# Kernel optimization log

Hardware: AMD Instinct MI355X
Metric: run time of the kernel (lower is better)

The kernel has to match this reference:

```python
import jax, jax.numpy as jnp
import numpy as np

HEADS = 4


def setup_inputs() -> dict:
    key = jax.random.key(0)
    kx, kqkv, kbq, ko, kbo = jax.random.split(key, 5)
    B, C, H, W = 4, 256, 64, 64
    x = jax.random.normal(kx, (B, C, H, W), dtype=jnp.float32)
    # torch nn.Linear stores weight as [out_features, in_features]
    w_qkv = jax.random.normal(kqkv, (3 * C, C), dtype=jnp.float32) * (1.0 / np.sqrt(C))
    b_qkv = jax.random.normal(kbq, (3 * C,), dtype=jnp.float32) * 0.02
    w_o = jax.random.normal(ko, (C, C), dtype=jnp.float32) * (1.0 / np.sqrt(C))
    b_o = jax.random.normal(kbo, (C,), dtype=jnp.float32) * 0.02
    return {"x": x, "w_qkv": w_qkv, "b_qkv": b_qkv, "w_o": w_o, "b_o": b_o}


def reference(x, w_qkv, b_qkv, w_o, b_o):
    B, C, H, W = x.shape
    S = H * W
    hd = C // HEADS
    # (B, C, H, W) -> (B, S, C)
    xt = x.reshape(B, C, S).transpose(0, 2, 1)
    qkv = xt @ w_qkv.T + b_qkv                      # (B, S, 3C)
    q, k, v = jnp.split(qkv, 3, axis=-1)
    def to_heads(t):
        return t.reshape(B, S, HEADS, hd).transpose(0, 2, 1, 3)  # (B, h, S, hd)
    q, k, v = to_heads(q), to_heads(k), to_heads(v)
    scores = jnp.einsum('bhqd,bhkd->bhqk', q, k) / jnp.sqrt(jnp.float32(hd))
    attn = jax.nn.softmax(scores, axis=-1)          # dropout inactive (eval)
    out = jnp.einsum('bhqk,bhkd->bhqd', attn, v)    # (B, h, S, hd)
    out = out.transpose(0, 2, 1, 3).reshape(B, S, C)
    y = out @ w_o.T + b_o                            # (B, S, C)
    y = y.reshape(B, H, W, C).transpose(0, 3, 1, 2)  # (B, C, H, W)
    return y
```

## Files before the change

### kernel.cpp

```cpp
#include <hip/hip_runtime.h>
#include <stdint.h>

#define DI __device__ __forceinline__

typedef __attribute__((ext_vector_type(8))) __bf16 bf16x8;
typedef __attribute__((ext_vector_type(8))) unsigned short u16x8;
typedef __attribute__((ext_vector_type(4))) float f32x4;
typedef __attribute__((ext_vector_type(4))) uint32_t u32x4;
typedef unsigned short u16;

constexpr int Bb = 4, Cc = 256, Ss = 4096, HD = 64;
constexpr int ELEMS = Bb * Cc * Ss;

DI float bf2f(u16 h) { union { unsigned u; float f; } x; x.u = ((unsigned)h) << 16; return x.f; }
DI u16 f2bf(float f) {
  union { float f; unsigned u; } x; x.f = f;
  return (u16)((x.u + 0x7FFFu + ((x.u >> 16) & 1u)) >> 16);
}
DI uint32_t pack2bf_trunc(float a, float b) {
  union { float f; uint32_t u; } xa, xb;
  xa.f = a; xb.f = b;
  return __builtin_amdgcn_perm(xb.u, xa.u, 0x07060302u);
}
DI bf16x8 ldfrag(const u16* p) { return __builtin_bit_cast(bf16x8, *(const u16x8*)p); }

DI void g2l16(const u16* g, u16* l) {
  __builtin_amdgcn_global_load_lds((const __attribute__((address_space(1))) uint32_t*)(const void*)g,
                                   (__attribute__((address_space(3))) uint32_t*)(void*)l, 16, 0, 0);
}

__global__ __launch_bounds__(256) void k_transpose(const float* __restrict__ x, u16* __restrict__ xt,
                                                   const float* __restrict__ wq, const float* __restrict__ wo,
                                                   u16* __restrict__ wqb, u16* __restrict__ wob) {
  __shared__ u16 T[64][72];
  const int st = blockIdx.x, ct = blockIdx.y, b = blockIdx.z;
  const int tid = threadIdx.x;
  {
    int flat = blockIdx.x + 64 * blockIdx.y + 256 * blockIdx.z;
    int widx = flat * 256 + tid;
    if (widx < 196608) wqb[widx] = f2bf(wq[widx]);
    else wob[widx - 196608] = f2bf(wo[widx - 196608]);
  }
#pragma unroll
  for (int e = 0; e < 2; e++) {
    int ss = tid + e * 256;
    int r = ss >> 3, seg = ss & 7;
    size_t base = ((size_t)(b * Cc + ct * 64 + r) << 12) + st * 64 + seg * 8;
    u16x8 t;
#pragma unroll
    for (int j = 0; j < 8; j++) t[j] = f2bf(x[base + j]);
    *(u16x8*)&T[r][(seg ^ ((r >> 3) & 7)) * 8] = t;
  }
  __syncthreads();
#pragma unroll
  for (int e = 0; e < 2; e++) {
    int ss = tid + e * 256;
    int sr = ss >> 3, cseg = ss & 7;
    u16x8 o;
#pragma unroll
    for (int j = 0; j < 8; j++) {
      int row = cseg * 8 + j;
      o[j] = T[row][(((sr >> 3) ^ cseg) * 8) + (sr & 7)];
    }
    *(u16x8*)(xt + ((size_t)(b * Ss + st * 64 + sr) << 8) + ct * 64 + cseg * 8) = o;
  }
}

DI void stage_tile(const u16* __restrict__ src, int pitch, int r0, int k0, u16 (*dst)[40], int tid) {
#pragma unroll
  for (int e = 0; e < 2; e++) {
    int c = tid + e * 256;
    int row = c >> 2, seg = c & 3;
    u16x8 t = *(const u16x8*)(src + (size_t)(r0 + row) * pitch + k0 + seg * 8);
    *(u16x8*)&dst[row][seg * 8] = t;
  }
}

__global__ __launch_bounds__(256) void k_qkv(const u16* __restrict__ xt, const u16* __restrict__ w,
                                             const float* __restrict__ bias,
                                             u16* __restrict__ q, u16* __restrict__ kk_, u16* __restrict__ vt) {
  __shared__ union {
    u16 ab[2][128][40];
    u16 vtile[128][132];
  } sm;
  const int tid = threadIdx.x;
  const int wv = tid >> 6, lane = tid & 63;
  const int wm = wv >> 1, wn = wv & 1;
  const int lr = lane & 15, quad = lane >> 4;
  const int r0 = blockIdx.x * 128;
  const int j0 = blockIdx.y * 128;
  f32x4 acc[4][4] = {};
  for (int k0 = 0; k0 < 256; k0 += 32) {
    __syncthreads();
    stage_tile(xt, 256, r0, k0, sm.ab[0], tid);
    stage_tile(w, 256, j0, k0, sm.ab[1], tid);
    __syncthreads();
    bf16x8 a[4], b[4];
#pragma unroll
    for (int mt = 0; mt < 4; mt++) a[mt] = ldfrag(&sm.ab[0][wm * 64 + mt * 16 + lr][quad * 8]);
#pragma unroll
    for (int nt = 0; nt < 4; nt++) b[nt] = ldfrag(&sm.ab[1][wn * 64 + nt * 16 + lr][quad * 8]);
#pragma unroll
    for (int mt = 0; mt < 4; mt++)
#pragma unroll
      for (int nt = 0; nt < 4; nt++)
        acc[mt][nt] = __builtin_amdgcn_mfma_f32_16x16x32_bf16(a[mt], b[nt], acc[mt][nt], 0, 0, 0);
  }
  if (blockIdx.y < 4) {
    const int part = blockIdx.y >> 1;
    u16* outp = part ? kk_ : q;
    const float sc = part ? 1.0f : 0.18033688f;
#pragma unroll
    for (int nt = 0; nt < 4; nt++) {
      int j = j0 + wn * 64 + nt * 16 + lr;
      float bj = bias[j];
      int cc = j & 255, head = cc >> 6, d = cc & 63;
#pragma unroll
      for (int mt = 0; mt < 4; mt++)
#pragma unroll
        for (int rg = 0; rg < 4; rg++) {
          int row = r0 + wm * 64 + mt * 16 + quad * 4 + rg;
          int b_ = row >> 12, s = row & 4095;
          outp[((size_t)((b_ * 4 + head) * Ss + s) << 6) + d] = f2bf((acc[mt][nt][rg] + bj) * sc);
        }
    }
  } else {
    const int hb = (blockIdx.y - 4) * 2;
    float bj[4];
#pragma unroll
    for (int nt = 0; nt < 4; nt++) bj[nt] = bias[j0 + wn * 64 + nt * 16 + lr];
    __syncthreads();
#pragma unroll
    for (int nt = 0; nt < 4; nt++) {
      int lc = wn * 64 + nt * 16 + lr;
#pragma unroll
      for (int mt = 0; mt < 4; mt++)
#pragma unroll
        for (int rg = 0; rg < 4; rg++)
          sm.vtile[wm * 64 + mt * 16 + quad * 4 + rg][lc] = f2bf(acc[mt][nt][rg] + bj[nt]);
    }
    __syncthreads();
    const int b2 = r0 >> 12, sbase = r0 & 4095;
#pragma unroll
    for (int it = 0; it < 8; it++) {
      int seg = tid + it * 256;
      int sq = seg & 15, hd = seg >> 4;
      int c = sq >> 3, s8 = sq & 7;
      u16x8 o;
#pragma unroll
      for (int j = 0; j < 8; j++) {
        int slot = s8 * 8 + j;
        int sw = (((slot >> 5) & 1) << 5) | (((slot >> 2) & 1) << 4) |
                 (((slot >> 3) & 3) << 2) | (slot & 3);
        o[j] = sm.vtile[c * 64 + sw][hd];
      }
      int head = hb + (hd >> 6), d = hd & 63;
      *(u16x8*)(vt + ((size_t)((b2 * 4 + head) * 64 + d) << 12) + sbase + c * 64 + s8 * 8) = o;
    }
  }
}

__global__ __launch_bounds__(512, 4) void k_attn(const u16* __restrict__ Q, const u16* __restrict__ K,
                                                 const u16* __restrict__ VT, u16* __restrict__ AO,
                                                 u16* __restrict__ AOP, float* __restrict__ lpart,
                                                 int nsplit) {
  __shared__ u16 Kl[2][64][64];
  __shared__ u16 Vl[2][64][64];
  const int tid = threadIdx.x;
  const int wv = tid >> 6, lane = tid & 63;
  const int lr = lane & 15, quad = lane >> 4;
  const int bh = blockIdx.y;
  const int b_ = bh >> 2, head = bh & 3;
  const int qbase = blockIdx.x * 256 + wv * 32;
  const int sp = blockIdx.z;
  const int nchunk = 64 / nsplit, kcg0 = sp * nchunk;
  const u16* Qh = Q + (size_t)bh * Ss * HD;
  const u16* Kh = K + (size_t)bh * Ss * HD;
  const u16* Vh = VT + (size_t)bh * HD * Ss;

  bf16x8 qb[2][2];
#pragma unroll
  for (int nt = 0; nt < 2; nt++)
#pragma unroll
    for (int ks = 0; ks < 2; ks++)
      qb[nt][ks] = ldfrag(Qh + (size_t)(qbase + nt * 16 + lr) * HD + ks * 32 + quad * 8);

  u16x8 ov;
#pragma unroll
  for (int j = 0; j < 8; j++) ov[j] = 0x3F80;
  const bf16x8 ones = __builtin_bit_cast(bf16x8, ov);

  f32x4 O[2][4] = {};
  f32x4 lacc[2] = {};

  const int srow = wv * 8 + (lane >> 3);
  const int sseg = ((lane & 7) ^ (lane >> 3)) * 8;
  const u16* pK = Kh + ((size_t)(kcg0 * 64 + srow) << 6) + sseg;
  const u16* pV = Vh + ((size_t)srow << 12) + kcg0 * 64 + sseg;
  auto stage = [&](int buf) {
    g2l16(pK, &Kl[buf][wv * 8][0]);
    g2l16(pV, &Vl[buf][wv * 8][0]);
    pK += 4096; pV += 64;
  };

  stage(0);
  __syncthreads();

  for (int kc = 0; kc < nchunk; kc++) {
    const int cur = kc & 1;
    if (kc + 1 < nchunk) stage(cur ^ 1);

    u32x4 pa[2][2];
#pragma unroll
    for (int t = 0; t < 4; t++) {
      const int krow = t * 16 + lr;
      bf16x8 ka0 = ldfrag(&Kl[cur][krow][(quad ^ (lr & 7)) * 8]);
      bf16x8 ka1 = ldfrag(&Kl[cur][krow][((4 + quad) ^ (lr & 7)) * 8]);
      f32x4 St[2] = {};
      __builtin_amdgcn_s_setprio(1);
#pragma unroll
      for (int nt = 0; nt < 2; nt++)
        St[nt] = __builtin_amdgcn_mfma_f32_16x16x32_bf16(ka0, qb[nt][0], St[nt], 0, 0, 0);
#pragma unroll
      for (int nt = 0; nt < 2; nt++)
        St[nt] = __builtin_amdgcn_mfma_f32_16x16x32_bf16(ka1, qb[nt][1], St[nt], 0, 0, 0);
      __builtin_amdgcn_s_setprio(0);
      const int h = t >> 1, k2 = (t & 1) * 2;
#pragma unroll
      for (int nt = 0; nt < 2; nt++) {
        float p0 = __builtin_amdgcn_exp2f(St[nt][0]);
        float p1 = __builtin_amdgcn_exp2f(St[nt][1]);
        float p2 = __builtin_amdgcn_exp2f(St[nt][2]);
        float p3 = __builtin_amdgcn_exp2f(St[nt][3]);
        pa[h][nt][k2] = pack2bf_trunc(p0, p1);
        pa[h][nt][k2 + 1] = pack2bf_trunc(p2, p3);
      }
    }
#pragma unroll
    for (int h = 0; h < 2; h++) {
#pragma unroll
      for (int dt = 0; dt < 4; dt++) {
        bf16x8 vb = ldfrag(&Vl[cur][dt * 16 + lr][((h * 4 + quad) ^ (lr & 7)) * 8]);
        __builtin_amdgcn_s_setprio(1);
#pragma unroll
        for (int mt = 0; mt < 2; mt++)
          O[mt][dt] = __builtin_amdgcn_mfma_f32_16x16x32_bf16(
              __builtin_bit_cast(bf16x8, pa[h][mt]), vb, O[mt][dt], 0, 0, 0);
        __builtin_amdgcn_s_setprio(0);
      }
#pragma unroll
      for (int mt = 0; mt < 2; mt++)
        lacc[mt] = __builtin_amdgcn_mfma_f32_16x16x32_bf16(
            __builtin_bit_cast(bf16x8, pa[h][mt]), ones, lacc[mt], 0, 0, 0);
    }
    __syncthreads();
  }

  u16* dst = (nsplit == 1) ? AO : (AOP + (size_t)sp * ELEMS);
  if (nsplit > 1 && lr == 0) {
    float* lp = lpart + (size_t)sp * (16 * Ss) + bh * Ss;
#pragma unroll
    for (int mt = 0; mt < 2; mt++)
#pragma unroll
      for (int rg = 0; rg < 4; rg++) lp[qbase + mt * 16 + quad * 4 + rg] = lacc[mt][rg];
  }
#pragma unroll
  for (int mt = 0; mt < 2; mt++)
#pragma unroll
    for (int rg = 0; rg < 4; rg++) {
      float inv = 1.0f / lacc[mt][rg];
      int s = qbase + mt * 16 + quad * 4 + rg;
#pragma unroll
      for (int dt = 0; dt < 4; dt++)
        dst[((size_t)(b_ * Ss + s) << 8) + head * 64 + dt * 16 + lr] = f2bf(O[mt][dt][rg] * inv);
    }
}

__global__ __launch_bounds__(256) void k_oproj(const u16* __restrict__ wo, const u16* __restrict__ ao,
                                               const u16* __restrict__ AOP, const float* __restrict__ lpart,
                                               const float* __restrict__ bo, float* __restrict__ y, int nsplit) {
  __shared__ u16 As[128][40], Bs[128][40];
  const int tid = threadIdx.x;
  const int wv = tid >> 6, lane = tid & 63;
  const int wm = wv >> 1, wn = wv & 1;
  const int lr = lane & 15, quad = lane >> 4;
  const int n0 = blockIdx.x * 128;
  const int m0 = blockIdx.y * 128;
  f32x4 acc[4][4] = {};
  for (int k0 = 0; k0 < 256; k0 += 32) {
    __syncthreads();
    stage_tile(wo, 256, m0, k0, As, tid);
#pragma unroll
    for (int e = 0; e < 2; e++) {
      int c = tid + e * 256;
      int row = c >> 2, seg = c & 3;
      int bs = n0 + row, cc = k0 + seg * 8;
      u16x8 t;
      if (nsplit == 1) {
        t = *(const u16x8*)(ao + ((size_t)bs << 8) + cc);
      } else {
        int b = bs >> 12, s = bs & 4095, head = cc >> 6;
        int li = (b * 4 + head) * Ss + s;
        float accv[8] = {0.f, 0.f, 0.f, 0.f, 0.f, 0.f, 0.f, 0.f};
        float lsum = 0.f;
        for (int spl = 0; spl < nsplit; spl++) {
          float l = lpart[(size_t)spl * (16 * Ss) + li];
          u16x8 a = *(const u16x8*)(AOP + (size_t)spl * ELEMS + ((size_t)bs << 8) + cc);
          lsum += l;
#pragma unroll
          for (int i = 0; i < 8; i++) accv[i] += l * bf2f(a[i]);
        }
        float inv = 1.0f / lsum;
#pragma unroll
        for (int i = 0; i < 8; i++) t[i] = f2bf(accv[i] * inv);
      }
      *(u16x8*)&Bs[row][seg * 8] = t;
    }
    __syncthreads();
    bf16x8 a[4], b[4];
#pragma unroll
    for (int mt = 0; mt < 4; mt++) a[mt] = ldfrag(&As[wm * 64 + mt * 16 + lr][quad * 8]);
#pragma unroll
    for (int nt = 0; nt < 4; nt++) b[nt] = ldfrag(&Bs[wn * 64 + nt * 16 + lr][quad * 8]);
#pragma unroll
    for (int mt = 0; mt < 4; mt++)
#pragma unroll
      for (int nt = 0; nt < 4; nt++)
        acc[mt][nt] = __builtin_amdgcn_mfma_f32_16x16x32_bf16(a[mt], b[nt], acc[mt][nt], 0, 0, 0);
  }
#pragma unroll
  for (int mt = 0; mt < 4; mt++)
#pragma unroll
    for (int rg = 0; rg < 4; rg++) {
      int c = m0 + wm * 64 + mt * 16 + quad * 4 + rg;
      float bc = bo[c];
#pragma unroll
      for (int nt = 0; nt < 4; nt++) {
        int col = n0 + wn * 64 + nt * 16 + lr;
        int b_ = col >> 12, s = col & 4095;
        y[((size_t)(b_ * Cc + c) << 12) + s] = acc[mt][nt][rg] + bc;
      }
    }
}

extern "C" void kernel_launch(void* const* d_in, const int* in_sizes, int n_in,
                              void* d_out, int out_size, void* d_ws, size_t ws_size,
                              hipStream_t stream) {
  const float* x = (const float*)d_in[0];
  const float* w_qkv = (const float*)d_in[1];
  const float* b_qkv = (const float*)d_in[2];
  const float* w_o = (const float*)d_in[3];
  const float* b_o = (const float*)d_in[4];
  float* y = (float*)d_out;
  u16* ws = (u16*)d_ws;
  u16* xt = ws;
  u16* q = ws + (size_t)ELEMS;
  u16* k = ws + (size_t)2 * ELEMS;
  u16* vt = ws + (size_t)3 * ELEMS;
  u16* ao = xt;
  u16* wqb = ws + (size_t)4 * ELEMS;
  u16* wob = wqb + 196608;
  const size_t Wu16 = (size_t)4 * ELEMS + 262144;
  auto need = [&](int n) { return (Wu16 + (size_t)n * ELEMS) * 2 + (size_t)n * 16 * Ss * 4; };
  const int nsplit = (ws_size >= need(2)) ? 2 : 1;
  u16* aop = ws + Wu16;
  float* lpart = (float*)(aop + (size_t)nsplit * ELEMS);

  k_transpose<<<dim3(64, 4, 4), 256, 0, stream>>>(x, xt, w_qkv, w_o, wqb, wob);
  k_qkv<<<dim3(128, 6), 256, 0, stream>>>(xt, wqb, b_qkv, q, k, vt);
  k_attn<<<dim3(16, 16, nsplit), 512, 0, stream>>>(q, k, vt, ao, aop, lpart, nsplit);
  k_oproj<<<dim3(128, 2), 256, 0, stream>>>(wob, ao, aop, lpart, b_o, y, nsplit);
}
```

Measured before the change: 177.1 us.

## Drop attention KV split, coalesce QKV stores, vectorize loads, retile out-proj

Removes the split-KV path from attention: each block now walks all 64 key chunks and writes normalized output directly, and out-projection no longer merges partial results. QKV epilogue for Q/K stages results through shared memory so stores become 16-byte vectors instead of scattered 2-byte writes. The transpose kernel reads x with float4 loads, and out-projection uses 64-row M tiles with twice as many blocks. Attention launches only 256 blocks, which may underfill the GPU where the split previously added parallelism, but the partial-output write and merge traffic is gone.

```diff
diff --git a/kernel.cpp b/kernel.cpp
--- a/kernel.cpp
+++ b/kernel.cpp
@@ -46,9 +46,11 @@
     int ss = tid + e * 256;
     int r = ss >> 3, seg = ss & 7;
     size_t base = ((size_t)(b * Cc + ct * 64 + r) << 12) + st * 64 + seg * 8;
+    const float4* xv = (const float4*)(x + base);
+    float4 v0 = xv[0], v1 = xv[1];
     u16x8 t;
-#pragma unroll
-    for (int j = 0; j < 8; j++) t[j] = f2bf(x[base + j]);
+    t[0] = f2bf(v0.x); t[1] = f2bf(v0.y); t[2] = f2bf(v0.z); t[3] = f2bf(v0.w);
+    t[4] = f2bf(v1.x); t[5] = f2bf(v1.y); t[6] = f2bf(v1.z); t[7] = f2bf(v1.w);
     *(u16x8*)&T[r][(seg ^ ((r >> 3) & 7)) * 8] = t;
   }
   __syncthreads();
@@ -81,7 +83,7 @@
                                              u16* __restrict__ q, u16* __restrict__ kk_, u16* __restrict__ vt) {
   __shared__ union {
     u16 ab[2][128][40];
-    u16 vtile[128][132];
+    u16 tile[128][136];
   } sm;
   const int tid = threadIdx.x;
   const int wv = tid >> 6, lane = tid & 63;
@@ -106,30 +108,36 @@
       for (int nt = 0; nt < 4; nt++)
         acc[mt][nt] = __builtin_amdgcn_mfma_f32_16x16x32_bf16(a[mt], b[nt], acc[mt][nt], 0, 0, 0);
   }
+  float bj[4];
+#pragma unroll
+  for (int nt = 0; nt < 4; nt++) bj[nt] = bias[j0 + wn * 64 + nt * 16 + lr];
+  __syncthreads();
   if (blockIdx.y < 4) {
     const int part = blockIdx.y >> 1;
     u16* outp = part ? kk_ : q;
     const float sc = part ? 1.0f : 0.18033688f;
 #pragma unroll
     for (int nt = 0; nt < 4; nt++) {
-      int j = j0 + wn * 64 + nt * 16 + lr;
-      float bj = bias[j];
-      int cc = j & 255, head = cc >> 6, d = cc & 63;
+      int lc = wn * 64 + nt * 16 + lr;
 #pragma unroll
       for (int mt = 0; mt < 4; mt++)
 #pragma unroll
-        for (int rg = 0; rg < 4; rg++) {
-          int row = r0 + wm * 64 + mt * 16 + quad * 4 + rg;
-          int b_ = row >> 12, s = row & 4095;
-          outp[((size_t)((b_ * 4 + head) * Ss + s) << 6) + d] = f2bf((acc[mt][nt][rg] + bj) * sc);
-        }
+        for (int rg = 0; rg < 4; rg++)
+          sm.tile[wm * 64 + mt * 16 + quad * 4 + rg][lc] = f2bf((acc[mt][nt][rg] + bj[nt]) * sc);
+    }
+    __syncthreads();
+    const int hb2 = (blockIdx.y & 1) * 2;
+#pragma unroll
+    for (int it = 0; it < 8; it++) {
+      int seg = tid + it * 256;
+      int row = seg >> 4, cs = seg & 15;
+      u16x8 o = *(const u16x8*)&sm.tile[row][cs * 8];
+      int head = hb2 + (cs >> 3), d0 = (cs & 7) * 8;
+      int rr = r0 + row, b_ = rr >> 12, s = rr & 4095;
+      *(u16x8*)(outp + ((size_t)((b_ * 4 + head) * Ss + s) << 6) + d0) = o;
     }
   } else {
     const int hb = (blockIdx.y - 4) * 2;
-    float bj[4];
-#pragma unroll
-    for (int nt = 0; nt < 4; nt++) bj[nt] = bias[j0 + wn * 64 + nt * 16 + lr];
-    __syncthreads();
 #pragma unroll
     for (int nt = 0; nt < 4; nt++) {
       int lc = wn * 64 + nt * 16 + lr;
@@ -137,7 +145,7 @@
       for (int mt = 0; mt < 4; mt++)
 #pragma unroll
         for (int rg = 0; rg < 4; rg++)
-          sm.vtile[wm * 64 + mt * 16 + quad * 4 + rg][lc] = f2bf(acc[mt][nt][rg] + bj[nt]);
+          sm.tile[wm * 64 + mt * 16 + quad * 4 + rg][lc] = f2bf(acc[mt][nt][rg] + bj[nt]);
     }
     __syncthreads();
     const int b2 = r0 >> 12, sbase = r0 & 4095;
@@ -152,7 +160,7 @@
         int slot = s8 * 8 + j;
         int sw = (((slot >> 5) & 1) << 5) | (((slot >> 2) & 1) << 4) |
                  (((slot >> 3) & 3) << 2) | (slot & 3);
-        o[j] = sm.vtile[c * 64 + sw][hd];
+        o[j] = sm.tile[c * 64 + sw][hd];
       }
       int head = hb + (hd >> 6), d = hd & 63;
       *(u16x8*)(vt + ((size_t)((b2 * 4 + head) * 64 + d) << 12) + sbase + c * 64 + s8 * 8) = o;
@@ -161,9 +169,7 @@
 }
 
 __global__ __launch_bounds__(512, 4) void k_attn(const u16* __restrict__ Q, const u16* __restrict__ K,
-                                                 const u16* __restrict__ VT, u16* __restrict__ AO,
-                                                 u16* __restrict__ AOP, float* __restrict__ lpart,
-                                                 int nsplit) {
+                                                 const u16* __restrict__ VT, u16* __restrict__ AO) {
   __shared__ u16 Kl[2][64][64];
   __shared__ u16 Vl[2][64][64];
   const int tid = threadIdx.x;
@@ -172,8 +178,6 @@
   const int bh = blockIdx.y;
   const int b_ = bh >> 2, head = bh & 3;
   const int qbase = blockIdx.x * 256 + wv * 32;
-  const int sp = blockIdx.z;
-  const int nchunk = 64 / nsplit, kcg0 = sp * nchunk;
   const u16* Qh = Q + (size_t)bh * Ss * HD;
   const u16* Kh = K + (size_t)bh * Ss * HD;
   const u16* Vh = VT + (size_t)bh * HD * Ss;
@@ -195,8 +199,8 @@
 
   const int srow = wv * 8 + (lane >> 3);
   const int sseg = ((lane & 7) ^ (lane >> 3)) * 8;
-  const u16* pK = Kh + ((size_t)(kcg0 * 64 + srow) << 6) + sseg;
-  const u16* pV = Vh + ((size_t)srow << 12) + kcg0 * 64 + sseg;
+  const u16* pK = Kh + ((size_t)srow << 6) + sseg;
+  const u16* pV = Vh + ((size_t)srow << 12) + sseg;
   auto stage = [&](int buf) {
     g2l16(pK, &Kl[buf][wv * 8][0]);
     g2l16(pV, &Vl[buf][wv * 8][0]);
@@ -206,9 +210,9 @@
   stage(0);
   __syncthreads();
 
-  for (int kc = 0; kc < nchunk; kc++) {
+  for (int kc = 0; kc < 64; kc++) {
     const int cur = kc & 1;
-    if (kc + 1 < nchunk) stage(cur ^ 1);
+    if (kc + 1 < 64) stage(cur ^ 1);
 
     u32x4 pa[2][2];
 #pragma unroll
@@ -256,14 +260,6 @@
     __syncthreads();
   }
 
-  u16* dst = (nsplit == 1) ? AO : (AOP + (size_t)sp * ELEMS);
-  if (nsplit > 1 && lr == 0) {
-    float* lp = lpart + (size_t)sp * (16 * Ss) + bh * Ss;
-#pragma unroll
-    for (int mt = 0; mt < 2; mt++)
-#pragma unroll
-      for (int rg = 0; rg < 4; rg++) lp[qbase + mt * 16 + quad * 4 + rg] = lacc[mt][rg];
-  }
 #pragma unroll
   for (int mt = 0; mt < 2; mt++)
 #pragma unroll
@@ -272,67 +268,49 @@
       int s = qbase + mt * 16 + quad * 4 + rg;
 #pragma unroll
       for (int dt = 0; dt < 4; dt++)
-        dst[((size_t)(b_ * Ss + s) << 8) + head * 64 + dt * 16 + lr] = f2bf(O[mt][dt][rg] * inv);
+        AO[((size_t)(b_ * Ss + s) << 8) + head * 64 + dt * 16 + lr] = f2bf(O[mt][dt][rg] * inv);
     }
 }
 
 __global__ __launch_bounds__(256) void k_oproj(const u16* __restrict__ wo, const u16* __restrict__ ao,
-                                               const u16* __restrict__ AOP, const float* __restrict__ lpart,
-                                               const float* __restrict__ bo, float* __restrict__ y, int nsplit) {
-  __shared__ u16 As[128][40], Bs[128][40];
+                                               const float* __restrict__ bo, float* __restrict__ y) {
+  __shared__ u16 As[64][40], Bs[128][40];
   const int tid = threadIdx.x;
   const int wv = tid >> 6, lane = tid & 63;
   const int wm = wv >> 1, wn = wv & 1;
   const int lr = lane & 15, quad = lane >> 4;
   const int n0 = blockIdx.x * 128;
-  const int m0 = blockIdx.y * 128;
-  f32x4 acc[4][4] = {};
+  const int m0 = blockIdx.y * 64;
+  f32x4 acc[2][4] = {};
   for (int k0 = 0; k0 < 256; k0 += 32) {
     __syncthreads();
-    stage_tile(wo, 256, m0, k0, As, tid);
+    {
+      int row = tid >> 2, seg = tid & 3;
+      *(u16x8*)&As[row][seg * 8] = *(const u16x8*)(wo + (m0 + row) * 256 + k0 + seg * 8);
+    }
 #pragma unroll
     for (int e = 0; e < 2; e++) {
       int c = tid + e * 256;
       int row = c >> 2, seg = c & 3;
-      int bs = n0 + row, cc = k0 + seg * 8;
-      u16x8 t;
-      if (nsplit == 1) {
-        t = *(const u16x8*)(ao + ((size_t)bs << 8) + cc);
-      } else {
-        int b = bs >> 12, s = bs & 4095, head = cc >> 6;
-        int li = (b * 4 + head) * Ss + s;
-        float accv[8] = {0.f, 0.f, 0.f, 0.f, 0.f, 0.f, 0.f, 0.f};
-        float lsum = 0.f;
-        for (int spl = 0; spl < nsplit; spl++) {
-          float l = lpart[(size_t)spl * (16 * Ss) + li];
-          u16x8 a = *(const u16x8*)(AOP + (size_t)spl * ELEMS + ((size_t)bs << 8) + cc);
-          lsum += l;
-#pragma unroll
-          for (int i = 0; i < 8; i++) accv[i] += l * bf2f(a[i]);
-        }
-        float inv = 1.0f / lsum;
-#pragma unroll
-        for (int i = 0; i < 8; i++) t[i] = f2bf(accv[i] * inv);
-      }
-      *(u16x8*)&Bs[row][seg * 8] = t;
-    }
-    __syncthreads();
-    bf16x8 a[4], b[4];
-#pragma unroll
-    for (int mt = 0; mt < 4; mt++) a[mt] = ldfrag(&As[wm * 64 + mt * 16 + lr][quad * 8]);
+      *(u16x8*)&Bs[row][seg * 8] = *(const u16x8*)(ao + ((size_t)(n0 + row) << 8) + k0 + seg * 8);
+    }
+    __syncthreads();
+    bf16x8 a[2], b[4];
+#pragma unroll
+    for (int mt = 0; mt < 2; mt++) a[mt] = ldfrag(&As[wm * 32 + mt * 16 + lr][quad * 8]);
 #pragma unroll
     for (int nt = 0; nt < 4; nt++) b[nt] = ldfrag(&Bs[wn * 64 + nt * 16 + lr][quad * 8]);
 #pragma unroll
-    for (int mt = 0; mt < 4; mt++)
+    for (int mt = 0; mt < 2; mt++)
 #pragma unroll
       for (int nt = 0; nt < 4; nt++)
         acc[mt][nt] = __builtin_amdgcn_mfma_f32_16x16x32_bf16(a[mt], b[nt], acc[mt][nt], 0, 0, 0);
   }
 #pragma unroll
-  for (int mt = 0; mt < 4; mt++)
+  for (int mt = 0; mt < 2; mt++)
 #pragma unroll
     for (int rg = 0; rg < 4; rg++) {
-      int c = m0 + wm * 64 + mt * 16 + quad * 4 + rg;
+      int c = m0 + wm * 32 + mt * 16 + quad * 4 + rg;
       float bc = bo[c];
 #pragma unroll
       for (int nt = 0; nt < 4; nt++) {
@@ -360,14 +338,9 @@
   u16* ao = xt;
   u16* wqb = ws + (size_t)4 * ELEMS;
   u16* wob = wqb + 196608;
-  const size_t Wu16 = (size_t)4 * ELEMS + 262144;
-  auto need = [&](int n) { return (Wu16 + (size_t)n * ELEMS) * 2 + (size_t)n * 16 * Ss * 4; };
-  const int nsplit = (ws_size >= need(2)) ? 2 : 1;
-  u16* aop = ws + Wu16;
-  float* lpart = (float*)(aop + (size_t)nsplit * ELEMS);
 
   k_transpose<<<dim3(64, 4, 4), 256, 0, stream>>>(x, xt, w_qkv, w_o, wqb, wob);
   k_qkv<<<dim3(128, 6), 256, 0, stream>>>(xt, wqb, b_qkv, q, k, vt);
-  k_attn<<<dim3(16, 16, nsplit), 512, 0, stream>>>(q, k, vt, ao, aop, lpart, nsplit);
-  k_oproj<<<dim3(128, 2), 256, 0, stream>>>(wob, ao, aop, lpart, b_o, y, nsplit);
-}
+  k_attn<<<dim3(16, 16), 512, 0, stream>>>(q, k, vt, ao);
+  k_oproj<<<dim3(128, 4), 256, 0, stream>>>(wob, ao, b_o, y);
+}
```

After: 191.5 us. +8.1%, slower.
